# Kernel tuning notes

Measured on AMD Instinct MI355X. Metric: run time of the kernel, lower is better.

The kernel has to match this reference:

```python
import jax, jax.numpy as jnp
import numpy as np

NUM_CLASSES = 10  # CINIC-10


def setup_inputs() -> dict:
    key = jax.random.key(0)
    k1, k2 = jax.random.split(key)
    embeddings = jax.random.normal(k1, (131072, 512), dtype=jnp.float32)
    labels = jax.random.randint(k2, (131072,), 0, NUM_CLASSES)
    return {"embeddings": embeddings, "labels": labels}


def reference(embeddings, labels):
    # Per-class mean (prototypes) as a segment reduction. With all classes
    # present, torch.unique(labels) == [0..9] sorted, so the remapped
    # target_indices equal labels directly.
    n = embeddings.shape[0]
    sums = jax.ops.segment_sum(embeddings, labels, num_segments=NUM_CLASSES)  # [C, d]
    counts = jax.ops.segment_sum(jnp.ones((n,), embeddings.dtype), labels,
                                 num_segments=NUM_CLASSES)                    # [C]
    prototypes = sums / counts[:, None]

    # Squared Euclidean distances: ||e||^2 + ||p||^2 - 2 e.p  (== cdist(...)**2)
    sq_e = jnp.sum(embeddings * embeddings, axis=1, keepdims=True)  # [B, 1]
    sq_p = jnp.sum(prototypes * prototypes, axis=1)                 # [C]
    d2 = sq_e + sq_p[None, :] - 2.0 * (embeddings @ prototypes.T)   # [B, C]
    d2 = jnp.maximum(d2, 0.0)

    logits = -d2
    logp = jax.nn.log_softmax(logits, axis=-1)
    loss = -jnp.mean(jnp.take_along_axis(logp, labels[:, None], axis=1))
    return (loss, logits)
```

## Files before the change

kernel.cpp:

```cpp
#include <hip/hip_runtime.h>

#define NROWS   131072
#define DIMS    512
#define NC      10
#define NCOPY   32
#define SUMSTRIDE 5120

typedef __attribute__((ext_vector_type(8))) short short8;
typedef __attribute__((ext_vector_type(4))) float floatx4;


static __device__ __forceinline__ unsigned int pk2(float lo, float hi) {
    return (__float_as_uint(hi) & 0xFFFF0000u) | (__float_as_uint(lo) >> 16);
}

static __device__ __forceinline__ short8 pack8(const float4 a, const float4 b) {
    union { unsigned int u[4]; short8 v; } r;
    r.u[0] = pk2(a.x, a.y);
    r.u[1] = pk2(a.z, a.w);
    r.u[2] = pk2(b.x, b.y);
    r.u[3] = pk2(b.z, b.w);
    return r.v;
}


__global__ __launch_bounds__(256) void k_seg(const float* __restrict__ E,
                                             const int* __restrict__ L,
                                             float* __restrict__ sums,
                                             int* __restrict__ counts) {
    __shared__ float red[NC * DIMS];
    __shared__ int lc[16];
    const int tid  = threadIdx.x;
    const int half = tid >> 7;
    const int dt   = tid & 127;
    if (tid < 16) lc[tid] = 0;
    __syncthreads();

    const int rows0 = blockIdx.x * 256;
    const float4* Ev = (const float4*)E;

    float4 z = {0.f, 0.f, 0.f, 0.f};
    float4 a0=z,a1=z,a2=z,a3=z,a4=z,a5=z,a6=z,a7=z,a8=z,a9=z;

    int idx = (rows0 + half) * 128 + dt;
    float4 v = Ev[idx];
    int lab = L[rows0 + half];

    for (int i = 0; i < 128; ++i) {
        float4 vn = v; int ln = lab;
        if (i < 127) {
            vn = Ev[idx + 256];
            ln = L[rows0 + 2 * i + 2 + half];
            idx += 256;
        }
        if (dt == 0) atomicAdd(&lc[lab], 1);
        switch (lab) {
            case 0: a0.x+=v.x; a0.y+=v.y; a0.z+=v.z; a0.w+=v.w; break;
            case 1: a1.x+=v.x; a1.y+=v.y; a1.z+=v.z; a1.w+=v.w; break;
            case 2: a2.x+=v.x; a2.y+=v.y; a2.z+=v.z; a2.w+=v.w; break;
            case 3: a3.x+=v.x; a3.y+=v.y; a3.z+=v.z; a3.w+=v.w; break;
            case 4: a4.x+=v.x; a4.y+=v.y; a4.z+=v.z; a4.w+=v.w; break;
            case 5: a5.x+=v.x; a5.y+=v.y; a5.z+=v.z; a5.w+=v.w; break;
            case 6: a6.x+=v.x; a6.y+=v.y; a6.z+=v.z; a6.w+=v.w; break;
            case 7: a7.x+=v.x; a7.y+=v.y; a7.z+=v.z; a7.w+=v.w; break;
            case 8: a8.x+=v.x; a8.y+=v.y; a8.z+=v.z; a8.w+=v.w; break;
            default: a9.x+=v.x; a9.y+=v.y; a9.z+=v.z; a9.w+=v.w; break;
        }
        v = vn; lab = ln;
    }

    float4* R = (float4*)red;
    if (half) {
        R[0*128+dt]=a0; R[1*128+dt]=a1; R[2*128+dt]=a2; R[3*128+dt]=a3;
        R[4*128+dt]=a4; R[5*128+dt]=a5; R[6*128+dt]=a6; R[7*128+dt]=a7;
        R[8*128+dt]=a8; R[9*128+dt]=a9;
    }
    __syncthreads();
    if (!half) {
        const int base = (blockIdx.x & (NCOPY - 1)) * SUMSTRIDE;
        float4 t;
#define MERGE_ATOM(c, ac)                                                     \
        t = R[(c)*128 + dt];                                                  \
        ac.x += t.x; ac.y += t.y; ac.z += t.z; ac.w += t.w;                   \
        { float* d = &sums[base + (c)*512 + 4*dt];                            \
          atomicAdd(d+0, ac.x); atomicAdd(d+1, ac.y);                         \
          atomicAdd(d+2, ac.z); atomicAdd(d+3, ac.w); }
        MERGE_ATOM(0,a0) MERGE_ATOM(1,a1) MERGE_ATOM(2,a2) MERGE_ATOM(3,a3)
        MERGE_ATOM(4,a4) MERGE_ATOM(5,a5) MERGE_ATOM(6,a6) MERGE_ATOM(7,a7)
        MERGE_ATOM(8,a8) MERGE_ATOM(9,a9)
#undef MERGE_ATOM
    }
    if (tid < 16) {
        const int base = (blockIdx.x & (NCOPY - 1)) * 16;
        atomicAdd(&counts[base + tid], lc[tid]);
    }
}


__global__ __launch_bounds__(256) void k_proto(const float* __restrict__ sums,
                                               const int* __restrict__ counts,
                                               float* __restrict__ p2) {
    const int e = blockIdx.x * 256 + threadIdx.x;
    const int c = e >> 9;
    float val = 0.f;
    if (c < NC) {
        float s = 0.f; int n = 0;
        for (int cp = 0; cp < NCOPY; ++cp) {
            s += sums[cp * SUMSTRIDE + e];
            n += counts[cp * 16 + c];
        }
        val = 2.f * s / (float)n;
    }
    p2[e] = val;
}


__global__ __launch_bounds__(512) void k_pn(const float* __restrict__ p2,
                                            float* __restrict__ pn) {
    const int w = threadIdx.x >> 6, lane = threadIdx.x & 63;
    const float4* P = (const float4*)p2;
    for (int s = 0; s < 2; ++s) {
        const int c = w + s * 8;
        float4 a = P[c * 128 + lane * 2];
        float4 b = P[c * 128 + lane * 2 + 1];
        float ss = a.x*a.x + a.y*a.y + a.z*a.z + a.w*a.w
                 + b.x*b.x + b.y*b.y + b.z*b.z + b.w*b.w;
        ss += __shfl_xor(ss, 1);  ss += __shfl_xor(ss, 2);
        ss += __shfl_xor(ss, 4);  ss += __shfl_xor(ss, 8);
        ss += __shfl_xor(ss, 16); ss += __shfl_xor(ss, 32);
        if (lane == 0) pn[c] = 0.25f * ss;
    }
}


__global__ __launch_bounds__(256) void k_main(const float* __restrict__ E,
                                              const int* __restrict__ L,
                                              const float* __restrict__ p2,
                                              const float* __restrict__ pn,
                                              float* __restrict__ out) {
    const int tid  = threadIdx.x;
    const int wid  = tid >> 6, lane = tid & 63;
    const int c16  = lane & 15, quad = lane >> 4;

    short8 bf[16];
    const float4* P = (const float4*)p2;
#pragma unroll
    for (int kt = 0; kt < 16; ++kt) {
        float4 a = P[c16 * 128 + kt * 8 + quad * 2];
        float4 b = P[c16 * 128 + kt * 8 + quad * 2 + 1];
        bf[kt] = pack8(a, b);
    }
    const float pnc = pn[c16];

    float lossp = 0.f;
    const int gw = blockIdx.x * 4 + wid;
    for (int t = gw; t < 8192; t += 4096) {
        const int tile  = 8191 - t;
        const int rbase = tile * 16;
        const float4* A = (const float4*)(E + (rbase + c16) * DIMS);

        floatx4 acc = {0.f, 0.f, 0.f, 0.f};
        float nrm = 0.f;
#pragma unroll
        for (int kt = 0; kt < 16; ++kt) {
            float4 a = A[kt * 8 + quad * 2];
            float4 b = A[kt * 8 + quad * 2 + 1];
            nrm += a.x*a.x + a.y*a.y + a.z*a.z + a.w*a.w;
            nrm += b.x*b.x + b.y*b.y + b.z*b.z + b.w*b.w;
            acc = __builtin_amdgcn_mfma_f32_16x16x32_bf16(pack8(a, b), bf[kt],
                                                          acc, 0, 0, 0);
        }
        nrm += __shfl_xor(nrm, 16);
        nrm += __shfl_xor(nrm, 32);

#pragma unroll
        for (int i = 0; i < 4; ++i) {
            const int row = rbase + quad * 4 + i;
            const float nr = __shfl(nrm, quad * 4 + i);
            float lg = acc[i] - nr - pnc;
            lg = fminf(lg, 0.f);
            float ml = (c16 < NC) ? lg : -3.0e38f;
            ml = fmaxf(ml, __shfl_xor(ml, 1));
            ml = fmaxf(ml, __shfl_xor(ml, 2));
            ml = fmaxf(ml, __shfl_xor(ml, 4));
            ml = fmaxf(ml, __shfl_xor(ml, 8));
            float ex = (c16 < NC) ? __expf(lg - ml) : 0.f;
            ex += __shfl_xor(ex, 1);
            ex += __shfl_xor(ex, 2);
            ex += __shfl_xor(ex, 4);
            ex += __shfl_xor(ex, 8);
            const float lse = ml + __logf(ex);
            if (c16 < NC) out[1 + row * NC + c16] = lg;
            const int lab = L[row];
            if (c16 == lab) lossp += lse - lg;
        }
    }

    lossp += __shfl_xor(lossp, 1);  lossp += __shfl_xor(lossp, 2);
    lossp += __shfl_xor(lossp, 4);  lossp += __shfl_xor(lossp, 8);
    lossp += __shfl_xor(lossp, 16); lossp += __shfl_xor(lossp, 32);
    __shared__ float ls[4];
    if (lane == 0) ls[wid] = lossp;
    __syncthreads();
    if (tid == 0)
        atomicAdd(out, (ls[0] + ls[1] + ls[2] + ls[3]) * (1.0f / (float)NROWS));
}


extern "C" void kernel_launch(void* const* d_in, const int* in_sizes, int n_in,
                              void* d_out, int out_size, void* d_ws, size_t ws_size,
                              hipStream_t stream) {
    const float* E = (const float*)d_in[0];
    const int*   L = (const int*)d_in[1];
    float* out = (float*)d_out;
    char* ws = (char*)d_ws;

    float* sums   = (float*)ws;
    int*   counts = (int*)(ws + 655360);
    float* p2     = (float*)(ws + 657408);
    float* pn     = (float*)(ws + 690176);

    (void)hipMemsetAsync(d_ws, 0, 657408, stream);
    (void)hipMemsetAsync(d_out, 0, sizeof(float), stream);

    k_seg  <<<NROWS / 256, 256, 0, stream>>>(E, L, sums, counts);
    k_proto<<<32,          256, 0, stream>>>(sums, counts, p2);
    k_pn   <<<1,           512, 0, stream>>>(p2, pn);
    k_main <<<1024,        256, 0, stream>>>(E, L, p2, pn, out);
}
```

Measured before the change: 475.0 us.

## Replace global atomic segment sums with per-block partials and tree reduction

The segment-sum kernel now uses 1024-thread blocks over 512 blocks. Each block reduces its 8 row-groups through LDS atomics and writes a private partial slab, so global atomics and the two memsets go away. A new two-stage reduction (k_red, then a fused k_pp that also computes counts, prototypes and norms and zeroes the loss) replaces k_proto and k_pn. k_main gets an occupancy hint and a reduced unroll. The cost is an extra 10 MB of partial-sum traffic and one single-block kernel on the critical path.

Result: slower. 550.1 us (+15.8%).

```diff
diff --git a/kernel.cpp b/kernel.cpp
--- a/kernel.cpp
+++ b/kernel.cpp
@@ -3,7 +3,7 @@
 #define NROWS   131072
 #define DIMS    512
 #define NC      10
-#define NCOPY   32
+#define SEG_BLOCKS 512
 #define SUMSTRIDE 5120
 
 typedef __attribute__((ext_vector_type(8))) short short8;
@@ -24,15 +24,16 @@
 }
 
 
-__global__ __launch_bounds__(256) void k_seg(const float* __restrict__ E,
-                                             const int* __restrict__ L,
-                                             float* __restrict__ sums,
-                                             int* __restrict__ counts) {
-    __shared__ float red[NC * DIMS];
+__global__ __launch_bounds__(1024, 4) void k_seg(const float* __restrict__ E,
+                                                 const int* __restrict__ L,
+                                                 float* __restrict__ part,
+                                                 int* __restrict__ counts) {
+    __shared__ float red[4 * NC * 128];
     __shared__ int lc[16];
-    const int tid  = threadIdx.x;
-    const int half = tid >> 7;
-    const int dt   = tid & 127;
+    const int tid   = threadIdx.x;
+    const int part8 = tid >> 7;
+    const int dt    = tid & 127;
+    for (int j = tid; j < 4 * NC * 128; j += 1024) red[j] = 0.f;
     if (tid < 16) lc[tid] = 0;
     __syncthreads();
 
@@ -42,16 +43,16 @@
     float4 z = {0.f, 0.f, 0.f, 0.f};
     float4 a0=z,a1=z,a2=z,a3=z,a4=z,a5=z,a6=z,a7=z,a8=z,a9=z;
 
-    int idx = (rows0 + half) * 128 + dt;
+    int idx = (rows0 + part8) * 128 + dt;
     float4 v = Ev[idx];
-    int lab = L[rows0 + half];
-
-    for (int i = 0; i < 128; ++i) {
+    int lab = L[rows0 + part8];
+
+    for (int i = 0; i < 32; ++i) {
         float4 vn = v; int ln = lab;
-        if (i < 127) {
-            vn = Ev[idx + 256];
-            ln = L[rows0 + 2 * i + 2 + half];
-            idx += 256;
+        if (i < 31) {
+            vn = Ev[idx + 1024];
+            ln = L[rows0 + 8 * i + 8 + part8];
+            idx += 1024;
         }
         if (dt == 0) atomicAdd(&lc[lab], 1);
         switch (lab) {
@@ -69,60 +70,99 @@
         v = vn; lab = ln;
     }
 
-    float4* R = (float4*)red;
-    if (half) {
-        R[0*128+dt]=a0; R[1*128+dt]=a1; R[2*128+dt]=a2; R[3*128+dt]=a3;
-        R[4*128+dt]=a4; R[5*128+dt]=a5; R[6*128+dt]=a6; R[7*128+dt]=a7;
-        R[8*128+dt]=a8; R[9*128+dt]=a9;
-    }
-    __syncthreads();
-    if (!half) {
-        const int base = (blockIdx.x & (NCOPY - 1)) * SUMSTRIDE;
-        float4 t;
-#define MERGE_ATOM(c, ac)                                                     \
-        t = R[(c)*128 + dt];                                                  \
-        ac.x += t.x; ac.y += t.y; ac.z += t.z; ac.w += t.w;                   \
-        { float* d = &sums[base + (c)*512 + 4*dt];                            \
-          atomicAdd(d+0, ac.x); atomicAdd(d+1, ac.y);                         \
-          atomicAdd(d+2, ac.z); atomicAdd(d+3, ac.w); }
-        MERGE_ATOM(0,a0) MERGE_ATOM(1,a1) MERGE_ATOM(2,a2) MERGE_ATOM(3,a3)
-        MERGE_ATOM(4,a4) MERGE_ATOM(5,a5) MERGE_ATOM(6,a6) MERGE_ATOM(7,a7)
-        MERGE_ATOM(8,a8) MERGE_ATOM(9,a9)
-#undef MERGE_ATOM
-    }
-    if (tid < 16) {
-        const int base = (blockIdx.x & (NCOPY - 1)) * 16;
-        atomicAdd(&counts[base + tid], lc[tid]);
-    }
-}
-
-
-__global__ __launch_bounds__(256) void k_proto(const float* __restrict__ sums,
-                                               const int* __restrict__ counts,
-                                               float* __restrict__ p2) {
-    const int e = blockIdx.x * 256 + threadIdx.x;
-    const int c = e >> 9;
-    float val = 0.f;
-    if (c < NC) {
-        float s = 0.f; int n = 0;
-        for (int cp = 0; cp < NCOPY; ++cp) {
-            s += sums[cp * SUMSTRIDE + e];
-            n += counts[cp * 16 + c];
-        }
-        val = 2.f * s / (float)n;
-    }
-    p2[e] = val;
-}
-
-
-__global__ __launch_bounds__(512) void k_pn(const float* __restrict__ p2,
-                                            float* __restrict__ pn) {
-    const int w = threadIdx.x >> 6, lane = threadIdx.x & 63;
-    const float4* P = (const float4*)p2;
-    for (int s = 0; s < 2; ++s) {
-        const int c = w + s * 8;
-        float4 a = P[c * 128 + lane * 2];
-        float4 b = P[c * 128 + lane * 2 + 1];
+    for (int j = 0; j < 10; ++j) {
+        int c = j + part8; if (c >= 10) c -= 10;
+        float4 ac;
+        switch (c) {
+            case 0: ac = a0; break; case 1: ac = a1; break;
+            case 2: ac = a2; break; case 3: ac = a3; break;
+            case 4: ac = a4; break; case 5: ac = a5; break;
+            case 6: ac = a6; break; case 7: ac = a7; break;
+            case 8: ac = a8; break; default: ac = a9; break;
+        }
+        atomicAdd(&red[0 * 1280 + c * 128 + dt], ac.x);
+        atomicAdd(&red[1 * 1280 + c * 128 + dt], ac.y);
+        atomicAdd(&red[2 * 1280 + c * 128 + dt], ac.z);
+        atomicAdd(&red[3 * 1280 + c * 128 + dt], ac.w);
+    }
+    __syncthreads();
+
+    float* dst = part + blockIdx.x * SUMSTRIDE;
+    for (int j = tid; j < SUMSTRIDE; j += 1024) dst[j] = red[j];
+    if (tid < 16) counts[blockIdx.x * 16 + tid] = lc[tid];
+}
+
+
+__global__ __launch_bounds__(256) void k_red(const float* __restrict__ part,
+                                             float* __restrict__ psum8) {
+    __shared__ float m[128];
+    const int t   = threadIdx.x;
+    const int col = t & 127, kh = t >> 7;
+    const int cc  = blockIdx.x % 40;
+    const int kc  = blockIdx.x / 40;
+    const int e   = cc * 128 + col;
+
+    const float* base = part + (size_t)(kc * 64 + kh * 32) * SUMSTRIDE + e;
+    float s0=0.f, s1=0.f, s2=0.f, s3=0.f;
+    for (int j = 0; j < 32; j += 4) {
+        s0 += base[(j + 0) * SUMSTRIDE];
+        s1 += base[(j + 1) * SUMSTRIDE];
+        s2 += base[(j + 2) * SUMSTRIDE];
+        s3 += base[(j + 3) * SUMSTRIDE];
+    }
+    float s = (s0 + s1) + (s2 + s3);
+    if (kh) m[col] = s;
+    __syncthreads();
+    if (!kh) psum8[kc * SUMSTRIDE + e] = s + m[col];
+}
+
+
+__global__ __launch_bounds__(512) void k_pp(const float* __restrict__ psum8,
+                                            const int* __restrict__ counts,
+                                            float* __restrict__ p2,
+                                            float* __restrict__ pn,
+                                            float* __restrict__ out) {
+    __shared__ float P[16 * DIMS];
+    __shared__ int tmp[512];
+    __shared__ int cnt[16];
+    const int t = threadIdx.x;
+
+    {
+        const int c0 = t & 15, chunk = t >> 4;
+        int s = 0;
+        for (int j = 0; j < 16; ++j) s += counts[(chunk * 16 + j) * 16 + c0];
+        tmp[t] = s;
+    }
+    __syncthreads();
+    if (t < 16) {
+        int n = 0;
+        for (int ch = 0; ch < 32; ++ch) n += tmp[ch * 16 + t];
+        cnt[t] = n;
+    }
+    if (t == 0) out[0] = 0.f;
+    __syncthreads();
+
+    for (int e = t; e < 16 * DIMS; e += 512) {
+        const int c = e >> 9, d = e & 511;
+        float val = 0.f;
+        if (c < NC) {
+            const int e2 = (d & 3) * 1280 + c * 128 + (d >> 2);
+            float s = 0.f;
+#pragma unroll
+            for (int j = 0; j < 8; ++j) s += psum8[j * SUMSTRIDE + e2];
+            val = 2.f * s / (float)cnt[c];
+        }
+        p2[e] = val;
+        P[e] = val;
+    }
+    __syncthreads();
+
+    const int w = t >> 6, lane = t & 63;
+    const float4* Pv = (const float4*)P;
+    for (int sdx = 0; sdx < 2; ++sdx) {
+        const int c = w + sdx * 8;
+        float4 a = Pv[c * 128 + lane * 2];
+        float4 b = Pv[c * 128 + lane * 2 + 1];
         float ss = a.x*a.x + a.y*a.y + a.z*a.z + a.w*a.w
                  + b.x*b.x + b.y*b.y + b.z*b.z + b.w*b.w;
         ss += __shfl_xor(ss, 1);  ss += __shfl_xor(ss, 2);
@@ -133,11 +173,11 @@
 }
 
 
-__global__ __launch_bounds__(256) void k_main(const float* __restrict__ E,
-                                              const int* __restrict__ L,
-                                              const float* __restrict__ p2,
-                                              const float* __restrict__ pn,
-                                              float* __restrict__ out) {
+__global__ __launch_bounds__(256, 3) void k_main(const float* __restrict__ E,
+                                                 const int* __restrict__ L,
+                                                 const float* __restrict__ p2,
+                                                 const float* __restrict__ pn,
+                                                 float* __restrict__ out) {
     const int tid  = threadIdx.x;
     const int wid  = tid >> 6, lane = tid & 63;
     const int c16  = lane & 15, quad = lane >> 4;
@@ -157,11 +197,11 @@
     for (int t = gw; t < 8192; t += 4096) {
         const int tile  = 8191 - t;
         const int rbase = tile * 16;
-        const float4* A = (const float4*)(E + (rbase + c16) * DIMS);
+        const float4* A = (const float4*)(E + (size_t)(rbase + c16) * DIMS);
 
         floatx4 acc = {0.f, 0.f, 0.f, 0.f};
         float nrm = 0.f;
-#pragma unroll
+#pragma unroll 4
         for (int kt = 0; kt < 16; ++kt) {
             float4 a = A[kt * 8 + quad * 2];
             float4 b = A[kt * 8 + quad * 2 + 1];
@@ -215,16 +255,14 @@
     float* out = (float*)d_out;
     char* ws = (char*)d_ws;
 
-    float* sums   = (float*)ws;
-    int*   counts = (int*)(ws + 655360);
-    float* p2     = (float*)(ws + 657408);
-    float* pn     = (float*)(ws + 690176);
-
-    (void)hipMemsetAsync(d_ws, 0, 657408, stream);
-    (void)hipMemsetAsync(d_out, 0, sizeof(float), stream);
-
-    k_seg  <<<NROWS / 256, 256, 0, stream>>>(E, L, sums, counts);
-    k_proto<<<32,          256, 0, stream>>>(sums, counts, p2);
-    k_pn   <<<1,           512, 0, stream>>>(p2, pn);
-    k_main <<<1024,        256, 0, stream>>>(E, L, p2, pn, out);
-}
+    float* part   = (float*)ws;
+    float* psum8  = (float*)(ws + 10485760);
+    int*   counts = (int*)  (ws + 10649600);
+    float* p2     = (float*)(ws + 10682368);
+    float* pn     = (float*)(ws + 10715136);
+
+    k_seg <<<SEG_BLOCKS, 1024, 0, stream>>>(E, L, part, counts);
+    k_red <<<320,         256, 0, stream>>>(part, psum8);
+    k_pp  <<<1,           512, 0, stream>>>(psum8, counts, p2, pn, out);
+    k_main<<<1024,        256, 0, stream>>>(E, L, p2, pn, out);
+}
```
